# Optimization experiments

Hardware: AMD Instinct MI355X
Metric: run time of the kernel (lower is better)

Reference implementation:

```python
import jax, jax.numpy as jnp
import numpy as np

N_NODES = 100000
N_EDGES = 1600000
IN_FEATS = 128
H1, H2 = 100, 200
OUT_FEATS = 64


def _glorot(key, shape):
    fan_in, fan_out = shape
    limit = float(np.sqrt(6.0 / (fan_in + fan_out)))
    return jax.random.uniform(key, shape, jnp.float32, -limit, limit)


def setup_inputs() -> dict:
    key = jax.random.key(0)
    ks = jax.random.split(key, 9)
    x = jax.random.normal(ks[0], (N_NODES, IN_FEATS), jnp.float32)
    edge_src = jax.random.randint(ks[1], (N_EDGES,), 0, N_NODES, jnp.int32)
    edge_dst = jax.random.randint(ks[2], (N_EDGES,), 0, N_NODES, jnp.int32)
    W1 = _glorot(ks[3], (IN_FEATS, H1)); b1 = jnp.zeros((H1,), jnp.float32)
    W2 = _glorot(ks[4], (H1, H2));       b2 = jnp.zeros((H2,), jnp.float32)
    W3 = _glorot(ks[5], (H2, OUT_FEATS)); b3 = jnp.zeros((OUT_FEATS,), jnp.float32)
    return {"x": x, "edge_src": edge_src, "edge_dst": edge_dst,
            "W1": W1, "b1": b1, "W2": W2, "b2": b2, "W3": W3, "b3": b3}


def _gcn_layer(h, src, dst, norm_src, norm_dst, W, b):
    # DGL GraphConv, norm='both': D_out^{-1/2} applied at src, sum-aggregate,
    # D_in^{-1/2} at dst, then dense linear + bias.
    h = h * norm_src[:, None]
    msgs = h[src]                                   # [E, d] gather
    agg = jax.ops.segment_sum(msgs, dst, num_segments=N_NODES)  # scatter-add
    agg = agg * norm_dst[:, None]
    return agg @ W + b


def reference(x, edge_src, edge_dst, W1, b1, W2, b2, W3, b3):
    ones = jnp.ones((N_EDGES,), jnp.float32)
    deg_out = jax.ops.segment_sum(ones, edge_src, num_segments=N_NODES)
    deg_in = jax.ops.segment_sum(ones, edge_dst, num_segments=N_NODES)
    norm_src = jax.lax.rsqrt(jnp.maximum(deg_out, 1.0))
    norm_dst = jax.lax.rsqrt(jnp.maximum(deg_in, 1.0))

    h = _gcn_layer(x, edge_src, edge_dst, norm_src, norm_dst, W1, b1)
    h = jax.nn.elu(h)
    h = _gcn_layer(h, edge_src, edge_dst, norm_src, norm_dst, W2, b2)
    h = jax.nn.elu(h)
    h = _gcn_layer(h, edge_src, edge_dst, norm_src, norm_dst, W3, b3)
    return jax.nn.sigmoid(h)
```

## Files before the change

kernel.cpp:

```cpp
#include <hip/hip_runtime.h>
#include <hip/hip_bf16.h>
#include <math.h>

#define NN 100000
#define NE 1600000

#define NBUCK 8
#define BSZ (NN / NBUCK)
#define CHUNKS 64
#define CH_E (NE / CHUNKS)

#define SCAN_BLK 256
#define NB_SCAN ((NN + SCAN_BLK - 1) / SCAN_BLK)

typedef float f32x4 __attribute__((ext_vector_type(4)));
typedef short s16x8 __attribute__((ext_vector_type(8)));
typedef unsigned short u16x4 __attribute__((ext_vector_type(4)));
typedef int i32x4 __attribute__((ext_vector_type(4)));

static inline int grid_for(long total, int block, long cap = 16384) {
    long b = (total + block - 1) / block;
    if (b > cap) b = cap;
    if (b < 1) b = 1;
    return (int)b;
}

__device__ __forceinline__ unsigned short f2b(float f) {
    __hip_bfloat16 h = __float2bfloat16(f);
    return __builtin_bit_cast(unsigned short, h);
}
__device__ __forceinline__ float b2f(unsigned short u) {
    unsigned int x = ((unsigned int)u) << 16;
    return __builtin_bit_cast(float, x);
}


__global__ __launch_bounds__(256) void partial_hist_kernel(
    const int* __restrict__ src, const int* __restrict__ dst,
    int* __restrict__ scratch)
{
    __shared__ int h[BSZ];
    int g = blockIdx.x & 7, c = blockIdx.x >> 3;
    int lo = g * BSZ;
    for (int i = threadIdx.x; i < BSZ; i += 256) h[i] = 0;
    __syncthreads();
    const i32x4* src4 = reinterpret_cast<const i32x4*>(src + c * CH_E);
    const i32x4* dst4 = reinterpret_cast<const i32x4*>(dst + c * CH_E);
    for (int i = threadIdx.x; i < CH_E / 4; i += 256) {
        i32x4 s4 = src4[i];
        i32x4 d4 = dst4[i];
#pragma unroll
        for (int j = 0; j < 4; ++j) {
            unsigned si = (unsigned)(s4[j] - lo);
            unsigned di = (unsigned)(d4[j] - lo);
            if (si < BSZ) atomicAdd(&h[si], 1);
            if (di < BSZ) atomicAdd(&h[di], 0x10000);
        }
    }
    __syncthreads();
    int* o = scratch + ((size_t)g * CHUNKS + c) * BSZ;
    for (int i = threadIdx.x; i < BSZ; i += 256) o[i] = h[i];
}

__global__ void reduce_hist_kernel(const int* __restrict__ scratch,
                                   float* __restrict__ ns, float* __restrict__ nd,
                                   int* __restrict__ cnt_dst) {
    int n = blockIdx.x * blockDim.x + threadIdx.x;
    if (n >= NN) return;
    int g = n / BSZ, i = n - g * BSZ;
    const int* p = scratch + (size_t)g * CHUNKS * BSZ + i;
    unsigned cs = 0, cd = 0;
#pragma unroll 8
    for (int c = 0; c < CHUNKS; ++c) {
        unsigned v = (unsigned)p[(size_t)c * BSZ];
        cs += v & 0xffffu;
        cd += v >> 16;
    }
    ns[n] = rsqrtf(fmaxf((float)cs, 1.0f));
    nd[n] = rsqrtf(fmaxf((float)cd, 1.0f));
    cnt_dst[n] = (int)cd;
}

__global__ void block_sum_kernel(const int* __restrict__ cnt, int* __restrict__ partials) {
    __shared__ int sm[SCAN_BLK];
    int i = blockIdx.x * SCAN_BLK + threadIdx.x;
    sm[threadIdx.x] = (i < NN) ? cnt[i] : 0;
    __syncthreads();
    for (int s = SCAN_BLK / 2; s > 0; s >>= 1) {
        if (threadIdx.x < s) sm[threadIdx.x] += sm[threadIdx.x + s];
        __syncthreads();
    }
    if (threadIdx.x == 0) partials[blockIdx.x] = sm[0];
}

__global__ void scan_partials_kernel(int* __restrict__ p) {
    __shared__ int sm[512];
    int tid = threadIdx.x;
    int v = (tid < NB_SCAN) ? p[tid] : 0;
    sm[tid] = v;
    __syncthreads();
    for (int off = 1; off < 512; off <<= 1) {
        int t = (tid >= off) ? sm[tid - off] : 0;
        __syncthreads();
        sm[tid] += t;
        __syncthreads();
    }
    if (tid < NB_SCAN) p[tid] = sm[tid] - v;
}

__global__ void block_scan_kernel(const int* __restrict__ cnt, const int* __restrict__ partials,
                                  int* __restrict__ row_ptr) {
    __shared__ int sm[SCAN_BLK];
    int i = blockIdx.x * SCAN_BLK + threadIdx.x;
    int v = (i < NN) ? cnt[i] : 0;
    sm[threadIdx.x] = v;
    __syncthreads();
    for (int off = 1; off < SCAN_BLK; off <<= 1) {
        int t = (threadIdx.x >= off) ? sm[threadIdx.x - off] : 0;
        __syncthreads();
        sm[threadIdx.x] += t;
        __syncthreads();
    }
    if (i < NN) {
        int excl = partials[blockIdx.x] + sm[threadIdx.x] - v;
        row_ptr[i] = excl;
        if (i == NN - 1) row_ptr[NN] = excl + v;
    }
}

__global__ void chunk_offs_kernel(int* __restrict__ scratch, const int* __restrict__ row_ptr) {
    int n = blockIdx.x * blockDim.x + threadIdx.x;
    if (n >= NN) return;
    int g = n / BSZ, i = n - g * BSZ;
    int* pd = scratch + (size_t)g * CHUNKS * BSZ + i;
    int base = row_ptr[n];
#pragma unroll 8
    for (int c = 0; c < CHUNKS; ++c) {
        unsigned cnt = ((unsigned)pd[(size_t)c * BSZ]) >> 16;
        pd[(size_t)c * BSZ] = base;
        base += (int)cnt;
    }
}

__global__ __launch_bounds__(256) void fill_chunked_kernel(
    const int* __restrict__ src, const int* __restrict__ dst,
    const int* __restrict__ scratch, int* __restrict__ col_src)
{
    __shared__ int off[BSZ];
    int g = blockIdx.x & 7, c = blockIdx.x >> 3;
    int lo = g * BSZ;
    const int* pd = scratch + ((size_t)g * CHUNKS + c) * BSZ;
    for (int i = threadIdx.x; i < BSZ; i += 256) off[i] = pd[i];
    __syncthreads();
    const i32x4* src4 = reinterpret_cast<const i32x4*>(src + c * CH_E);
    const i32x4* dst4 = reinterpret_cast<const i32x4*>(dst + c * CH_E);
    for (int i = threadIdx.x; i < CH_E / 4; i += 256) {
        i32x4 s4 = src4[i];
        i32x4 d4 = dst4[i];
#pragma unroll
        for (int j = 0; j < 4; ++j) {
            unsigned di = (unsigned)(d4[j] - lo);
            if (di < BSZ) {
                int p = atomicAdd(&off[di], 1);
                col_src[p] = s4[j];
            }
        }
    }
}


template <int K_REAL, int N_REAL, int NTILES>
__global__ void repack_kernel(const float* __restrict__ W, unsigned short* __restrict__ Wf,
                              int total) {
    int t = blockIdx.x * blockDim.x + threadIdx.x;
    if (t >= total) return;
    int j = t & 7, lane = (t >> 3) & 63, frag = t >> 9;
    int kt = frag / NTILES, nt = frag - kt * NTILES;
    int k = kt * 32 + (lane >> 4) * 8 + j;
    int n = nt * 16 + (lane & 15);
    float v = (k < K_REAL && n < N_REAL) ? W[(size_t)k * N_REAL + n] : 0.0f;
    Wf[t] = f2b(v);
}

__global__ void padbias_kernel(const float* __restrict__ b, float* __restrict__ bp,
                               int nreal, int npad) {
    int t = blockIdx.x * blockDim.x + threadIdx.x;
    if (t < npad) bp[t] = (t < nreal) ? b[t] : 0.0f;
}

template <int K_STEPS, int NTILES, int N_REAL, int EPI, int K_PAD, int AMODE>
__global__ __launch_bounds__(256) void gemm_kernel(
    const void* __restrict__ Aptr, const unsigned short* __restrict__ Wf,
    const float* __restrict__ rowscale, const float* __restrict__ bias,
    void* __restrict__ outv)
{
    int wave = blockIdx.x * (blockDim.x >> 6) + (threadIdx.x >> 6);
    int row0 = wave << 4;
    if (row0 >= NN) return;
    int lane = threadIdx.x & 63;
    int r = lane & 15, half = lane >> 4;

    f32x4 acc[NTILES];
#pragma unroll
    for (int nt = 0; nt < NTILES; ++nt) acc[nt] = (f32x4)(0.0f);

#pragma unroll
    for (int kt = 0; kt < K_STEPS; ++kt) {
        s16x8 a;
        if (AMODE == 0) {
            const unsigned short* arow = (const unsigned short*)Aptr
                + (size_t)(row0 + r) * K_PAD + half * 8 + kt * 32;
            a = *reinterpret_cast<const s16x8*>(arow);
        } else {
            const float* arow = (const float*)Aptr
                + (size_t)(row0 + r) * K_PAD + half * 8 + kt * 32;
            f32x4 alo = *reinterpret_cast<const f32x4*>(arow);
            f32x4 ahi = *reinterpret_cast<const f32x4*>(arow + 4);
#pragma unroll
            for (int j = 0; j < 4; ++j) {
                a[j]     = (short)f2b(alo[j]);
                a[4 + j] = (short)f2b(ahi[j]);
            }
        }
#pragma unroll
        for (int nt = 0; nt < NTILES; ++nt) {
            s16x8 b = *reinterpret_cast<const s16x8*>(
                Wf + (((kt * NTILES + nt) << 9) | (lane << 3)));
            acc[nt] = __builtin_amdgcn_mfma_f32_16x16x32_bf16(a, b, acc[nt], 0, 0, 0);
        }
    }

    int colbase = lane & 15;
    float rs[4];
#pragma unroll
    for (int j = 0; j < 4; ++j) rs[j] = rowscale[row0 + half * 4 + j];

    if (EPI == 2) {
        unsigned short* out = (unsigned short*)outv;
#pragma unroll
        for (int nt = 0; nt < NTILES; ++nt) {
            int col = nt * 16 + colbase;
            if (col < N_REAL) {
#pragma unroll
                for (int j = 0; j < 4; ++j) {
                    int row = row0 + half * 4 + j;
                    out[(size_t)row * N_REAL + col] = f2b(acc[nt][j] * rs[j]);
                }
            }
        }
    } else {
        unsigned short* out = (unsigned short*)outv;
        const int NOUT = NTILES * 16;
#pragma unroll
        for (int nt = 0; nt < NTILES; ++nt) {
            int col = nt * 16 + colbase;
            float bv = bias[col];
#pragma unroll
            for (int j = 0; j < 4; ++j) {
                int row = row0 + half * 4 + j;
                float v = acc[nt][j] * rs[j] + bv;
                v = (v > 0.0f) ? v : expm1f(v);
                out[(size_t)row * NOUT + col] = f2b(v);
            }
        }
    }
}


#define GACC4(yb, stride)                                                        \
    int i = start;                                                               \
    f32x4 a0 = (f32x4)(0.0f), a1 = (f32x4)(0.0f), a2 = (f32x4)(0.0f),            \
          a3 = (f32x4)(0.0f);                                                    \
    for (; i + 4 <= end; i += 4) {                                               \
        int s0 = col_src[i], s1 = col_src[i + 1];                                \
        int s2 = col_src[i + 2], s3 = col_src[i + 3];                            \
        u16x4 v0 = *reinterpret_cast<const u16x4*>(yb + (size_t)s0 * stride + g * 4); \
        u16x4 v1 = *reinterpret_cast<const u16x4*>(yb + (size_t)s1 * stride + g * 4); \
        u16x4 v2 = *reinterpret_cast<const u16x4*>(yb + (size_t)s2 * stride + g * 4); \
        u16x4 v3 = *reinterpret_cast<const u16x4*>(yb + (size_t)s3 * stride + g * 4); \
        _Pragma("unroll")                                                        \
        for (int j = 0; j < 4; ++j) {                                            \
            a0[j] += b2f(v0[j]); a1[j] += b2f(v1[j]);                            \
            a2[j] += b2f(v2[j]); a3[j] += b2f(v3[j]);                            \
        }                                                                        \
    }                                                                            \
    for (; i < end; ++i) {                                                       \
        int s0 = col_src[i];                                                     \
        u16x4 v0 = *reinterpret_cast<const u16x4*>(yb + (size_t)s0 * stride + g * 4); \
        _Pragma("unroll")                                                        \
        for (int j = 0; j < 4; ++j) a0[j] += b2f(v0[j]);                         \
    }                                                                            \
    f32x4 acc;                                                                   \
    _Pragma("unroll")                                                            \
    for (int j = 0; j < 4; ++j) acc[j] = (a0[j] + a1[j]) + (a2[j] + a3[j]);

__global__ void gather1_kernel(const unsigned short* __restrict__ y, const int* __restrict__ row_ptr,
                               const int* __restrict__ col_src, const float* __restrict__ ns,
                               const float* __restrict__ nd, const float* __restrict__ bias,
                               unsigned short* __restrict__ out) {
    unsigned t = blockIdx.x * blockDim.x + threadIdx.x;
    if (t >= NN * 25u) return;
    unsigned n = t / 25u, g = t - n * 25u;
    int start = row_ptr[n], end = row_ptr[n + 1];
    GACC4(y, 100)
    f32x4 b4 = *reinterpret_cast<const f32x4*>(bias + g * 4);
    float ndv = nd[n], nsv = ns[n];
    u16x4 o;
#pragma unroll
    for (int j = 0; j < 4; ++j) {
        float v = acc[j] * ndv + b4[j];
        v = (v > 0.0f) ? v : expm1f(v);
        o[j] = f2b(v * nsv);
    }
    *reinterpret_cast<u16x4*>(out + (size_t)n * 100 + g * 4) = o;
}

__global__ void gather2_kernel(const unsigned short* __restrict__ y, const int* __restrict__ row_ptr,
                               const int* __restrict__ col_src, unsigned short* __restrict__ out) {
    unsigned t = blockIdx.x * blockDim.x + threadIdx.x;
    if (t >= NN * 32u) return;
    unsigned n = t >> 5, g = t & 31u;
    if (g >= 25u) {
        u16x4 z = (u16x4)(0);
        *reinterpret_cast<u16x4*>(out + (size_t)n * 128 + 100 + (g - 25u) * 4) = z;
        return;
    }
    int start = row_ptr[n], end = row_ptr[n + 1];
    GACC4(y, 100)
    u16x4 o;
#pragma unroll
    for (int j = 0; j < 4; ++j) o[j] = f2b(acc[j]);
    *reinterpret_cast<u16x4*>(out + (size_t)n * 128 + g * 4) = o;
}

__global__ void gather3_kernel(const unsigned short* __restrict__ y, const int* __restrict__ row_ptr,
                               const int* __restrict__ col_src, const float* __restrict__ nd,
                               const float* __restrict__ bias, float* __restrict__ out) {
    unsigned t = blockIdx.x * blockDim.x + threadIdx.x;
    if (t >= NN * 16u) return;
    unsigned n = t >> 4, g = t & 15u;
    int start = row_ptr[n], end = row_ptr[n + 1];
    GACC4(y, 64)
    f32x4 b4 = *reinterpret_cast<const f32x4*>(bias + g * 4);
    float ndv = nd[n];
    f32x4 o;
#pragma unroll
    for (int j = 0; j < 4; ++j) {
        float v = acc[j] * ndv + b4[j];
        o[j] = 1.0f / (1.0f + expf(-v));
    }
    *reinterpret_cast<f32x4*>(out + (size_t)n * 64 + g * 4) = o;
}


extern "C" void kernel_launch(void* const* d_in, const int* in_sizes, int n_in,
                              void* d_out, int out_size, void* d_ws, size_t ws_size,
                              hipStream_t stream) {
    const float* x    = (const float*)d_in[0];
    const int*   esrc = (const int*)d_in[1];
    const int*   edst = (const int*)d_in[2];
    const float* W1   = (const float*)d_in[3];
    const float* b1   = (const float*)d_in[4];
    const float* W2   = (const float*)d_in[5];
    const float* b2   = (const float*)d_in[6];
    const float* W3   = (const float*)d_in[7];
    const float* b3   = (const float*)d_in[8];
    float* out = (float*)d_out;

    char* base = (char*)d_ws;
    size_t off = 0;
    auto alloc = [&](size_t bytes) -> void* {
        void* p = base + off;
        off += (bytes + 255) & ~(size_t)255;
        return p;
    };
    void* region1 = alloc((size_t)NN * 128 * 2);
    void* region2 = alloc((size_t)NN * 224 * 2);
    void* region3 = alloc((size_t)NN * 100 * 2);
    float* ns       = (float*)alloc(NN * 4);
    float* nd       = (float*)alloc(NN * 4);
    int*   cnt_dst  = (int*)alloc(NN * 4);
    int*   row_ptr  = (int*)alloc((NN + 1) * 4);
    int*   col_src  = (int*)alloc((size_t)NE * 4);
    int*   partials = (int*)alloc(512 * 4);
    unsigned short* W1f = (unsigned short*)alloc(4 * 7 * 512 * 2);
    unsigned short* W2f = (unsigned short*)alloc(4 * 14 * 512 * 2);
    unsigned short* W3f = (unsigned short*)alloc(7 * 4 * 512 * 2);
    float* b2p = (float*)alloc(224 * 4);

    int* scratch          = (int*)region1;
    unsigned short* agg2b = (unsigned short*)region1;
    unsigned short* y3    = (unsigned short*)region1;
    unsigned short* y1    = (unsigned short*)region2;
    unsigned short* h2b   = (unsigned short*)region2;
    unsigned short* h1s   = (unsigned short*)region3;

    const int BLK = 256;
    const int GEMM_GRID = (NN / 16 + 3) / 4;

    partial_hist_kernel<<<NBUCK * CHUNKS, 256, 0, stream>>>(esrc, edst, scratch);
    reduce_hist_kernel<<<grid_for(NN, BLK), BLK, 0, stream>>>(scratch, ns, nd, cnt_dst);
    block_sum_kernel<<<NB_SCAN, SCAN_BLK, 0, stream>>>(cnt_dst, partials);
    scan_partials_kernel<<<1, 512, 0, stream>>>(partials);
    block_scan_kernel<<<NB_SCAN, SCAN_BLK, 0, stream>>>(cnt_dst, partials, row_ptr);
    chunk_offs_kernel<<<grid_for(NN, BLK), BLK, 0, stream>>>(scratch, row_ptr);
    fill_chunked_kernel<<<NBUCK * CHUNKS, 256, 0, stream>>>(esrc, edst, scratch, col_src);

    repack_kernel<128, 100, 7><<<grid_for(28 * 512, BLK), BLK, 0, stream>>>(W1, W1f, 28 * 512);
    repack_kernel<100, 200, 14><<<grid_for(56 * 512, BLK), BLK, 0, stream>>>(W2, W2f, 56 * 512);
    repack_kernel<200, 64, 4><<<grid_for(28 * 512, BLK), BLK, 0, stream>>>(W3, W3f, 28 * 512);
    padbias_kernel<<<1, 256, 0, stream>>>(b2, b2p, 200, 224);

    gemm_kernel<4, 7, 100, 2, 128, 1><<<GEMM_GRID, BLK, 0, stream>>>(x, W1f, ns, nullptr, y1);
    gather1_kernel<<<grid_for((long)NN * 25, BLK, 1 << 30), BLK, 0, stream>>>(
        y1, row_ptr, col_src, ns, nd, b1, h1s);

    gather2_kernel<<<grid_for((long)NN * 32, BLK, 1 << 30), BLK, 0, stream>>>(
        h1s, row_ptr, col_src, agg2b);
    gemm_kernel<4, 14, 200, 1, 128, 0><<<GEMM_GRID, BLK, 0, stream>>>(agg2b, W2f, nd, b2p, h2b);

    gemm_kernel<7, 4, 64, 2, 224, 0><<<GEMM_GRID, BLK, 0, stream>>>(h2b, W3f, ns, nullptr, y3);
    gather3_kernel<<<grid_for((long)NN * 16, BLK, 1 << 30), BLK, 0, stream>>>(
        y3, row_ptr, col_src, nd, b3, out);
}
```

Baseline: 416.4 us.

## Merge weight prep launches, co-schedule CSR fill with first GEMM, unroll gathers by 8

The three weight-repack kernels and the bias pad are folded into one prep kernel launched up front, cutting launch count. The CSR fill kernel and the first GEMM become one launch whose blocks pick their role from the block index, so the two independent jobs can run on the GPU at the same time. The gather accumulation loop is unrolled to 8 edges per iteration for more loads in flight. The fused kernel reserves the fill path's 50 KB shared-memory array for every block, including GEMM blocks, which may lower GEMM occupancy. The wider unroll raises register pressure.

```diff
diff --git a/kernel.cpp b/kernel.cpp
--- a/kernel.cpp
+++ b/kernel.cpp
@@ -9,6 +9,8 @@
 #define BSZ (NN / NBUCK)
 #define CHUNKS 64
 #define CH_E (NE / CHUNKS)
+#define FILL_BLOCKS (NBUCK * CHUNKS)
+#define GEMM_GRID ((NN / 16 + 3) / 4)
 
 #define SCAN_BLK 256
 #define NB_SCAN ((NN + SCAN_BLK - 1) / SCAN_BLK)
@@ -142,38 +144,10 @@
     }
 }
 
-__global__ __launch_bounds__(256) void fill_chunked_kernel(
-    const int* __restrict__ src, const int* __restrict__ dst,
-    const int* __restrict__ scratch, int* __restrict__ col_src)
-{
-    __shared__ int off[BSZ];
-    int g = blockIdx.x & 7, c = blockIdx.x >> 3;
-    int lo = g * BSZ;
-    const int* pd = scratch + ((size_t)g * CHUNKS + c) * BSZ;
-    for (int i = threadIdx.x; i < BSZ; i += 256) off[i] = pd[i];
-    __syncthreads();
-    const i32x4* src4 = reinterpret_cast<const i32x4*>(src + c * CH_E);
-    const i32x4* dst4 = reinterpret_cast<const i32x4*>(dst + c * CH_E);
-    for (int i = threadIdx.x; i < CH_E / 4; i += 256) {
-        i32x4 s4 = src4[i];
-        i32x4 d4 = dst4[i];
-#pragma unroll
-        for (int j = 0; j < 4; ++j) {
-            unsigned di = (unsigned)(d4[j] - lo);
-            if (di < BSZ) {
-                int p = atomicAdd(&off[di], 1);
-                col_src[p] = s4[j];
-            }
-        }
-    }
-}
-
 
 template <int K_REAL, int N_REAL, int NTILES>
-__global__ void repack_kernel(const float* __restrict__ W, unsigned short* __restrict__ Wf,
-                              int total) {
-    int t = blockIdx.x * blockDim.x + threadIdx.x;
-    if (t >= total) return;
+__device__ __forceinline__ void repack_one(const float* __restrict__ W,
+                                           unsigned short* __restrict__ Wf, int t) {
     int j = t & 7, lane = (t >> 3) & 63, frag = t >> 9;
     int kt = frag / NTILES, nt = frag - kt * NTILES;
     int k = kt * 32 + (lane >> 4) * 8 + j;
@@ -182,22 +156,35 @@
     Wf[t] = f2b(v);
 }
 
-__global__ void padbias_kernel(const float* __restrict__ b, float* __restrict__ bp,
-                               int nreal, int npad) {
+#define R1_N (28 * 512)
+#define R2_N (56 * 512)
+#define R3_N (28 * 512)
+
+__global__ void prep_kernel(const float* __restrict__ W1, unsigned short* __restrict__ W1f,
+                            const float* __restrict__ W2, unsigned short* __restrict__ W2f,
+                            const float* __restrict__ W3, unsigned short* __restrict__ W3f,
+                            const float* __restrict__ b2, float* __restrict__ b2p) {
     int t = blockIdx.x * blockDim.x + threadIdx.x;
-    if (t < npad) bp[t] = (t < nreal) ? b[t] : 0.0f;
+    if (t < R1_N) {
+        repack_one<128, 100, 7>(W1, W1f, t);
+    } else if (t < R1_N + R2_N) {
+        repack_one<100, 200, 14>(W2, W2f, t - R1_N);
+    } else if (t < R1_N + R2_N + R3_N) {
+        repack_one<200, 64, 4>(W3, W3f, t - R1_N - R2_N);
+    } else if (t < R1_N + R2_N + R3_N + 224) {
+        int i = t - R1_N - R2_N - R3_N;
+        b2p[i] = (i < 200) ? b2[i] : 0.0f;
+    }
 }
 
 template <int K_STEPS, int NTILES, int N_REAL, int EPI, int K_PAD, int AMODE>
-__global__ __launch_bounds__(256) void gemm_kernel(
-    const void* __restrict__ Aptr, const unsigned short* __restrict__ Wf,
-    const float* __restrict__ rowscale, const float* __restrict__ bias,
-    void* __restrict__ outv)
+__device__ __forceinline__ void gemm_body(
+    int wave, int lane, const void* __restrict__ Aptr,
+    const unsigned short* __restrict__ Wf, const float* __restrict__ rowscale,
+    const float* __restrict__ bias, void* __restrict__ outv)
 {
-    int wave = blockIdx.x * (blockDim.x >> 6) + (threadIdx.x >> 6);
     int row0 = wave << 4;
     if (row0 >= NN) return;
-    int lane = threadIdx.x & 63;
     int r = lane & 15, half = lane >> 4;
 
     f32x4 acc[NTILES];
@@ -266,11 +253,77 @@
     }
 }
 
-
-#define GACC4(yb, stride)                                                        \
+template <int K_STEPS, int NTILES, int N_REAL, int EPI, int K_PAD, int AMODE>
+__global__ __launch_bounds__(256) void gemm_kernel(
+    const void* __restrict__ Aptr, const unsigned short* __restrict__ Wf,
+    const float* __restrict__ rowscale, const float* __restrict__ bias,
+    void* __restrict__ outv)
+{
+    int wave = blockIdx.x * (blockDim.x >> 6) + (threadIdx.x >> 6);
+    gemm_body<K_STEPS, NTILES, N_REAL, EPI, K_PAD, AMODE>(
+        wave, threadIdx.x & 63, Aptr, Wf, rowscale, bias, outv);
+}
+
+__global__ __launch_bounds__(256) void fill_gemm1_kernel(
+    const int* __restrict__ src, const int* __restrict__ dst,
+    const int* __restrict__ scratch, int* __restrict__ col_src,
+    const float* __restrict__ x, const unsigned short* __restrict__ W1f,
+    const float* __restrict__ ns, unsigned short* __restrict__ y1)
+{
+    __shared__ int off[BSZ];
+    if (blockIdx.x < FILL_BLOCKS) {
+        int g = blockIdx.x & 7, c = blockIdx.x >> 3;
+        int lo = g * BSZ;
+        const int* pd = scratch + ((size_t)g * CHUNKS + c) * BSZ;
+        for (int i = threadIdx.x; i < BSZ; i += 256) off[i] = pd[i];
+        __syncthreads();
+        const i32x4* src4 = reinterpret_cast<const i32x4*>(src + c * CH_E);
+        const i32x4* dst4 = reinterpret_cast<const i32x4*>(dst + c * CH_E);
+        for (int i = threadIdx.x; i < CH_E / 4; i += 256) {
+            i32x4 s4 = src4[i];
+            i32x4 d4 = dst4[i];
+#pragma unroll
+            for (int j = 0; j < 4; ++j) {
+                unsigned di = (unsigned)(d4[j] - lo);
+                if (di < BSZ) {
+                    int p = atomicAdd(&off[di], 1);
+                    col_src[p] = s4[j];
+                }
+            }
+        }
+    } else {
+        int bid = blockIdx.x - FILL_BLOCKS;
+        int wave = bid * 4 + (threadIdx.x >> 6);
+        gemm_body<4, 7, 100, 2, 128, 1>(wave, threadIdx.x & 63, x, W1f, ns, nullptr, y1);
+    }
+}
+
+
+#define GACC8(yb, stride)                                                        \
     int i = start;                                                               \
     f32x4 a0 = (f32x4)(0.0f), a1 = (f32x4)(0.0f), a2 = (f32x4)(0.0f),            \
           a3 = (f32x4)(0.0f);                                                    \
+    for (; i + 8 <= end; i += 8) {                                               \
+        int s0 = col_src[i],     s1 = col_src[i + 1];                            \
+        int s2 = col_src[i + 2], s3 = col_src[i + 3];                            \
+        int s4 = col_src[i + 4], s5 = col_src[i + 5];                            \
+        int s6 = col_src[i + 6], s7 = col_src[i + 7];                            \
+        u16x4 v0 = *reinterpret_cast<const u16x4*>(yb + (size_t)s0 * stride + g * 4); \
+        u16x4 v1 = *reinterpret_cast<const u16x4*>(yb + (size_t)s1 * stride + g * 4); \
+        u16x4 v2 = *reinterpret_cast<const u16x4*>(yb + (size_t)s2 * stride + g * 4); \
+        u16x4 v3 = *reinterpret_cast<const u16x4*>(yb + (size_t)s3 * stride + g * 4); \
+        u16x4 v4 = *reinterpret_cast<const u16x4*>(yb + (size_t)s4 * stride + g * 4); \
+        u16x4 v5 = *reinterpret_cast<const u16x4*>(yb + (size_t)s5 * stride + g * 4); \
+        u16x4 v6 = *reinterpret_cast<const u16x4*>(yb + (size_t)s6 * stride + g * 4); \
+        u16x4 v7 = *reinterpret_cast<const u16x4*>(yb + (size_t)s7 * stride + g * 4); \
+        _Pragma("unroll")                                                        \
+        for (int j = 0; j < 4; ++j) {                                            \
+            a0[j] += b2f(v0[j]) + b2f(v4[j]);                                    \
+            a1[j] += b2f(v1[j]) + b2f(v5[j]);                                    \
+            a2[j] += b2f(v2[j]) + b2f(v6[j]);                                    \
+            a3[j] += b2f(v3[j]) + b2f(v7[j]);                                    \
+        }                                                                        \
+    }                                                                            \
     for (; i + 4 <= end; i += 4) {                                               \
         int s0 = col_src[i], s1 = col_src[i + 1];                                \
         int s2 = col_src[i + 2], s3 = col_src[i + 3];                            \
@@ -302,7 +355,7 @@
     if (t >= NN * 25u) return;
     unsigned n = t / 25u, g = t - n * 25u;
     int start = row_ptr[n], end = row_ptr[n + 1];
-    GACC4(y, 100)
+    GACC8(y, 100)
     f32x4 b4 = *reinterpret_cast<const f32x4*>(bias + g * 4);
     float ndv = nd[n], nsv = ns[n];
     u16x4 o;
@@ -326,7 +379,7 @@
         return;
     }
     int start = row_ptr[n], end = row_ptr[n + 1];
-    GACC4(y, 100)
+    GACC8(y, 100)
     u16x4 o;
 #pragma unroll
     for (int j = 0; j < 4; ++j) o[j] = f2b(acc[j]);
@@ -340,7 +393,7 @@
     if (t >= NN * 16u) return;
     unsigned n = t >> 4, g = t & 15u;
     int start = row_ptr[n], end = row_ptr[n + 1];
-    GACC4(y, 64)
+    GACC8(y, 64)
     f32x4 b4 = *reinterpret_cast<const f32x4*>(bias + g * 4);
     float ndv = nd[n];
     f32x4 o;
@@ -383,9 +436,9 @@
     int*   row_ptr  = (int*)alloc((NN + 1) * 4);
     int*   col_src  = (int*)alloc((size_t)NE * 4);
     int*   partials = (int*)alloc(512 * 4);
-    unsigned short* W1f = (unsigned short*)alloc(4 * 7 * 512 * 2);
-    unsigned short* W2f = (unsigned short*)alloc(4 * 14 * 512 * 2);
-    unsigned short* W3f = (unsigned short*)alloc(7 * 4 * 512 * 2);
+    unsigned short* W1f = (unsigned short*)alloc(R1_N * 2);
+    unsigned short* W2f = (unsigned short*)alloc(R2_N * 2);
+    unsigned short* W3f = (unsigned short*)alloc(R3_N * 2);
     float* b2p = (float*)alloc(224 * 4);
 
     int* scratch          = (int*)region1;
@@ -396,7 +449,9 @@
     unsigned short* h1s   = (unsigned short*)region3;
 
     const int BLK = 256;
-    const int GEMM_GRID = (NN / 16 + 3) / 4;
+
+    prep_kernel<<<grid_for(R1_N + R2_N + R3_N + 224, BLK), BLK, 0, stream>>>(
+        W1, W1f, W2, W2f, W3, W3f, b2, b2p);
 
     partial_hist_kernel<<<NBUCK * CHUNKS, 256, 0, stream>>>(esrc, edst, scratch);
     reduce_hist_kernel<<<grid_for(NN, BLK), BLK, 0, stream>>>(scratch, ns, nd, cnt_dst);
@@ -404,14 +459,10 @@
     scan_partials_kernel<<<1, 512, 0, stream>>>(partials);
     block_scan_kernel<<<NB_SCAN, SCAN_BLK, 0, stream>>>(cnt_dst, partials, row_ptr);
     chunk_offs_kernel<<<grid_for(NN, BLK), BLK, 0, stream>>>(scratch, row_ptr);
-    fill_chunked_kernel<<<NBUCK * CHUNKS, 256, 0, stream>>>(esrc, edst, scratch, col_src);
-
-    repack_kernel<128, 100, 7><<<grid_for(28 * 512, BLK), BLK, 0, stream>>>(W1, W1f, 28 * 512);
-    repack_kernel<100, 200, 14><<<grid_for(56 * 512, BLK), BLK, 0, stream>>>(W2, W2f, 56 * 512);
-    repack_kernel<200, 64, 4><<<grid_for(28 * 512, BLK), BLK, 0, stream>>>(W3, W3f, 28 * 512);
-    padbias_kernel<<<1, 256, 0, stream>>>(b2, b2p, 200, 224);
-
-    gemm_kernel<4, 7, 100, 2, 128, 1><<<GEMM_GRID, BLK, 0, stream>>>(x, W1f, ns, nullptr, y1);
+
+    fill_gemm1_kernel<<<FILL_BLOCKS + GEMM_GRID, 256, 0, stream>>>(
+        esrc, edst, scratch, col_src, x, W1f, ns, y1);
+
     gather1_kernel<<<grid_for((long)NN * 25, BLK, 1 << 30), BLK, 0, stream>>>(
         y1, row_ptr, col_src, ns, nd, b1, h1s);
 
```

New measurement: 399.7 us. 1.04x faster.
